# Kernel tuning notes

Measured on AMD Instinct MI355X. Metric: run time of the kernel, lower is better.

The kernel has to match this reference:

```python
import jax, jax.numpy as jnp
import numpy as np
from jax import lax

D_MODEL = 768
D_INNER = 1536   # expand * d_model
D_STATE = 16
D_CONV = 4
DT_RANK = 48     # ceil(768/16)
BATCH, SEQLEN = 2, 1024


def silu(x):
    return x * jax.nn.sigmoid(x)


def causal_conv1d(x, w, b):
    # x: (B, L, d)  w: (d, K) depthwise  b: (d,)
    # matches torch Conv1d(groups=d, padding=K-1)[..., :L]
    K = w.shape[1]
    L = x.shape[1]
    xp = jnp.pad(x, ((0, 0), (K - 1, 0), (0, 0)))
    out = b
    for k in range(K):
        out = out + xp[:, k:k + L, :] * w[:, k]
    return out


def mamba_branch(xz, conv_w, conv_b, x_proj_w, dt_proj_w, dt_bias, A_log, D):
    # xz: (B, L, 2*d_inner); faithful to mamba_inner_fn_no_out_proj
    x, z = jnp.split(xz, 2, axis=-1)
    x = silu(causal_conv1d(x, conv_w, conv_b))
    x_dbl = x @ x_proj_w.T                                  # (B,L,dt_rank+2N)
    dt, Bc, Cc = jnp.split(x_dbl, [DT_RANK, DT_RANK + D_STATE], axis=-1)
    delta = jax.nn.softplus(dt @ dt_proj_w.T + dt_bias)     # (B,L,d)
    A = -jnp.exp(A_log)                                     # (d,N)
    dA = jnp.exp(delta[..., None] * A)                      # (B,L,d,N)
    dBx = (delta * x)[..., None] * Bc[:, :, None, :]        # (B,L,d,N)

    def step(h, inp):
        da, dbx = inp
        h = da * h + dbx
        return h, h

    h0 = jnp.zeros((x.shape[0], x.shape[2], D_STATE), x.dtype)
    _, hs = lax.scan(step, h0, (jnp.swapaxes(dA, 0, 1), jnp.swapaxes(dBx, 0, 1)))
    y = jnp.einsum('lbdn,bln->bld', hs, Cc) + x * D         # (B,L,d)
    return y * silu(z)


def setup_inputs() -> dict:
    key = jax.random.key(0)
    ks = jax.random.split(key, 16)
    d, dm, n, r, K = D_INNER, D_MODEL, D_STATE, DT_RANK, D_CONV
    A_log = jnp.log(jnp.broadcast_to(jnp.arange(1, n + 1, dtype=jnp.float32), (d, n)))
    # faithful dt bias init: inverse-softplus of log-uniform dt in [1e-3, 1e-1]
    def dt_bias(k):
        dt = jnp.exp(jax.random.uniform(k, (d,)) * (np.log(0.1) - np.log(0.001)) + np.log(0.001))
        dt = jnp.clip(dt, 1e-4)
        return dt + jnp.log(-jnp.expm1(-dt))
    return {
        'hidden_states': jax.random.normal(ks[0], (BATCH, SEQLEN, dm), jnp.float32),
        'in_proj_w': jax.random.normal(ks[1], (2 * d, dm), jnp.float32) / np.sqrt(dm),
        'conv_w': jax.random.normal(ks[2], (d, K), jnp.float32) / np.sqrt(K),
        'conv_b': jax.random.normal(ks[3], (d,), jnp.float32) * 0.02,
        'x_proj_w': jax.random.normal(ks[4], (r + 2 * n, d), jnp.float32) / np.sqrt(d),
        'dt_proj_w': jax.random.uniform(ks[5], (d, r), jnp.float32, -r ** -0.5, r ** -0.5),
        'dt_proj_b': dt_bias(ks[6]),
        'A_log': A_log,
        'D': jnp.ones((d,), jnp.float32),
        'conv_w_b': jax.random.normal(ks[7], (d, K), jnp.float32) / np.sqrt(K),
        'conv_b_b': jax.random.normal(ks[8], (d,), jnp.float32) * 0.02,
        'x_proj_w_b': jax.random.normal(ks[9], (r + 2 * n, d), jnp.float32) / np.sqrt(d),
        'dt_proj_w_b': jax.random.uniform(ks[10], (d, r), jnp.float32, -r ** -0.5, r ** -0.5),
        'dt_proj_b_b': dt_bias(ks[11]),
        'A_b_log': A_log,
        'D_b': jnp.ones((d,), jnp.float32),
        'out_proj_w': jax.random.normal(ks[12], (dm, d), jnp.float32) / np.sqrt(d),
    }


def reference(hidden_states, in_proj_w, conv_w, conv_b, x_proj_w, dt_proj_w, dt_proj_b,
              A_log, D, conv_w_b, conv_b_b, x_proj_w_b, dt_proj_w_b, dt_proj_b_b,
              A_b_log, D_b, out_proj_w):
    # bimamba v2: forward scan + backward (flipped) scan, summed, then out_proj
    xz = hidden_states @ in_proj_w.T                        # (B,L,2*d_inner)
    out_f = mamba_branch(xz, conv_w, conv_b, x_proj_w, dt_proj_w, dt_proj_b, A_log, D)
    out_r = mamba_branch(xz[:, ::-1, :], conv_w_b, conv_b_b, x_proj_w_b,
                         dt_proj_w_b, dt_proj_b_b, A_b_log, D_b)[:, ::-1, :]
    return (out_f + out_r) @ out_proj_w.T                   # (B,L,d_model)
```

## Files before the change

### kernel.cpp

```cpp
#include <hip/hip_runtime.h>
#include <hip/hip_bf16.h>

#define LL 1024
#define DI 1536
#define N2 3072
#define ML 2048

typedef __attribute__((ext_vector_type(8))) short short8;
typedef __attribute__((ext_vector_type(4))) float f4;
typedef __attribute__((ext_vector_type(4))) float f32x4;

__device__ __forceinline__ ushort f2bf(float f) {
  union { float f; unsigned u; } v; v.f = f;
  unsigned u = v.u;
  u += 0x7fffu + ((u >> 16) & 1u);
  return (ushort)(u >> 16);
}
__device__ __forceinline__ float bf2f(ushort u) {
  union { unsigned i; float f; } w; w.i = ((unsigned)u) << 16; return w.f;
}

__device__ __forceinline__ void gload16(const ushort* g, ushort* l) {
  __builtin_amdgcn_global_load_lds(
      (const __attribute__((address_space(1))) unsigned int*)g,
      (__attribute__((address_space(3))) unsigned int*)l, 16, 0, 0);
}

struct CvtSeg { const float* s; ushort* d; int n4; };
struct Cvt5 { CvtSeg seg[5]; };

#define CVT_BLOCKS 5232

__global__ void k_cvt(Cvt5 p, int total4,
                      const float* __restrict__ wf, const float* __restrict__ wb,
                      ushort* __restrict__ dtw) {
  int bid = blockIdx.x;
  if (bid < CVT_BLOCKS) {
    int i = bid * 256 + threadIdx.x;
    if (i >= total4) return;
    int off = i, sidx = 0;
    while (sidx < 4 && off >= p.seg[sidx].n4) { off -= p.seg[sidx].n4; ++sidx; }
    f4 v = *(const f4*)(p.seg[sidx].s + (size_t)off * 4);
    ushort4 o;
    o.x = f2bf(v.x); o.y = f2bf(v.y); o.z = f2bf(v.z); o.w = f2bf(v.w);
    *(ushort4*)(p.seg[sidx].d + (size_t)off * 4) = o;
  } else {
    int i = (bid - CVT_BLOCKS) * 256 + threadIdx.x;
    int c = i & 63;
    int rr = i >> 6;
    int dir = rr / 1536;
    int r = rr - dir * 1536;
    const float* w = dir ? wb : wf;
    dtw[i] = (c < 48) ? f2bf(w[r * 48 + c]) : (ushort)0;
  }
}

template<int EPI, bool NGUARD, int KS>
__global__ __launch_bounds__(256)
void k_gemm(const ushort* __restrict__ A, const ushort* __restrict__ Bm,
            float* __restrict__ C, int M, int N, int K,
            const float* __restrict__ bias, const float* __restrict__ bias2,
            size_t sA, size_t sB, size_t sC, size_t sKs, int kLen) {
  const int dir = blockIdx.z;
  A += (size_t)dir * sA;
  Bm += (size_t)dir * sB;
  C += (size_t)dir * sC;
  const float* bp = (EPI == 1) ? (dir ? bias2 : bias) : nullptr;

  int n0, kOff, kEnd;
  if (KS > 1) {
    int yb_ = blockIdx.y;
    int nt = yb_ / KS, ks = yb_ - nt * KS;
    n0 = nt * 128;
    kOff = ks * kLen;
    kEnd = kOff + kLen;
    C += (size_t)ks * sKs;
  } else {
    n0 = blockIdx.y * 128;
    kOff = 0;
    kEnd = K;
  }

  __shared__ ushort As[128 * 32];
  __shared__ ushort Bs[128 * 32];
  const int tid = threadIdx.x;
  const int m0 = blockIdx.x * 128;
  const int wv = tid >> 6;
  const int lane = tid & 63;
  const int wr = (wv >> 1) * 64;
  const int wc = (wv & 1) * 64;
  const int lr = lane & 15;
  const int lk = lane >> 4;
  f32x4 acc[4][4] = {};
  for (int k0 = kOff; k0 < kEnd; k0 += 32) {
    #pragma unroll
    for (int i = 0; i < 2; ++i) {
      int e = (tid + i * 256) * 8;
      int r = e >> 5;
      int c = e & 31;
      gload16(A + (size_t)(m0 + r) * K + k0 + c, &As[(i * 256 + wv * 64) * 8]);
      gload16(Bm + (size_t)(n0 + r) * K + k0 + c, &Bs[(i * 256 + wv * 64) * 8]);
    }
    __syncthreads();
    short8 af[4], bfr[4];
    #pragma unroll
    for (int m = 0; m < 4; ++m) af[m] = *(const short8*)(&As[(wr + m*16 + lr) * 32 + lk*8]);
    #pragma unroll
    for (int n = 0; n < 4; ++n) bfr[n] = *(const short8*)(&Bs[(wc + n*16 + lr) * 32 + lk*8]);
    #pragma unroll
    for (int m = 0; m < 4; ++m)
      #pragma unroll
      for (int n = 0; n < 4; ++n)
        acc[m][n] = __builtin_amdgcn_mfma_f32_16x16x32_bf16(af[m], bfr[n], acc[m][n], 0, 0, 0);
    __syncthreads();
  }
  #pragma unroll
  for (int m = 0; m < 4; ++m) {
    int gr = m0 + wr + m * 16 + lk * 4;
    #pragma unroll
    for (int n = 0; n < 4; ++n) {
      int gc = n0 + wc + n * 16 + lr;
      if (NGUARD && gc >= N) continue;
      #pragma unroll
      for (int r = 0; r < 4; ++r) {
        float v = acc[m][n][r];
        if (EPI == 1) {
          v += bp[gc];
          v = (v > 20.f) ? v : log1pf(__expf(v));
        }
        C[(size_t)(gr + r) * N + gc] = v;
      }
    }
  }
}

__global__ void k_xred(const float* __restrict__ partial,
                       float* __restrict__ dtBC, ushort* __restrict__ dtbf) {
  int i = blockIdx.x * 256 + threadIdx.x;
  int dir = i / 40960;
  int rem = i - dir * 40960;
  int row = rem / 20;
  int c4 = rem - row * 20;
  f4 s = {0.f, 0.f, 0.f, 0.f};
  #pragma unroll
  for (int ks = 0; ks < 8; ++ks) {
    f4 v = *(const f4*)(partial + (((size_t)(dir * 8 + ks) * 2048 + row) * 80 + c4 * 4));
    s.x += v.x; s.y += v.y; s.z += v.z; s.w += v.w;
  }
  *(f4*)(dtBC + ((size_t)dir * 163840 + (size_t)row * 80 + c4 * 4)) = s;
  if (c4 < 16) {
    ushort4 u;
    if (c4 < 12) { u.x = f2bf(s.x); u.y = f2bf(s.y); u.z = f2bf(s.z); u.w = f2bf(s.w); }
    else { u.x = 0; u.y = 0; u.z = 0; u.w = 0; }
    *(ushort4*)(dtbf + ((size_t)dir * 131072 + (size_t)row * 64 + c4 * 4)) = u;
  }
}

__global__ void k_ored(const float* __restrict__ part, float* __restrict__ out) {
  int i = blockIdx.x * 256 + threadIdx.x;
  f4 s = {0.f, 0.f, 0.f, 0.f};
  #pragma unroll
  for (int ks = 0; ks < 4; ++ks) {
    f4 v = *(const f4*)(part + (size_t)ks * 1572864 + (size_t)i * 4);
    s.x += v.x; s.y += v.y; s.z += v.z; s.w += v.w;
  }
  *(f4*)(out + (size_t)i * 4) = s;
}

#define CONV_R 8
__global__ __launch_bounds__(192)
void k_conv2(const float* __restrict__ xz,
             const float* __restrict__ wf, const float* __restrict__ bf_,
             const float* __restrict__ wb, const float* __restrict__ bb_,
             ushort* __restrict__ xcbf) {
  int d4 = blockIdx.z * 192 + threadIdx.x;
  int b = blockIdx.y;
  int l0 = blockIdx.x * CONV_R;
  int d = d4 * 4;
  f4 w0[4], w1[4];
  #pragma unroll
  for (int c = 0; c < 4; ++c) {
    w0[c] = *(const f4*)(wf + (size_t)d * 4 + c * 4);
    w1[c] = *(const f4*)(wb + (size_t)d * 4 + c * 4);
  }
  f4 bias0 = *(const f4*)(bf_ + d);
  f4 bias1 = *(const f4*)(bb_ + d);
  f4 win[CONV_R + 6];
  #pragma unroll
  for (int j = 0; j < CONV_R + 6; ++j) {
    int t = l0 - 3 + j;
    if (t >= 0 && t < LL) {
      win[j] = *(const f4*)(xz + ((size_t)(b * LL + t)) * N2 + d);
    } else {
      f4 z = {0.f, 0.f, 0.f, 0.f};
      win[j] = z;
    }
  }
  #pragma unroll
  for (int i = 0; i < CONV_R; ++i) {
    int l = l0 + i;
    float a0[4], a1[4];
    #pragma unroll
    for (int c = 0; c < 4; ++c) { a0[c] = bias0[c]; a1[c] = bias1[c]; }
    #pragma unroll
    for (int k = 0; k < 4; ++k) {
      f4 xv0 = win[i + k];
      f4 xv1 = win[i + 3 + k];
      #pragma unroll
      for (int c = 0; c < 4; ++c) {
        a0[c] += xv0[c] * w0[c][k];
        a1[c] += xv1[c] * w1[c][3 - k];
      }
    }
    ushort4 o0, o1;
    #pragma unroll
    for (int c = 0; c < 4; ++c) {
      a0[c] = a0[c] / (1.f + __expf(-a0[c]));
      a1[c] = a1[c] / (1.f + __expf(-a1[c]));
    }
    o0.x = f2bf(a0[0]); o0.y = f2bf(a0[1]); o0.z = f2bf(a0[2]); o0.w = f2bf(a0[3]);
    o1.x = f2bf(a1[0]); o1.y = f2bf(a1[1]); o1.z = f2bf(a1[2]); o1.w = f2bf(a1[3]);
    *(ushort4*)(xcbf + ((size_t)(b * LL + l)) * DI + d) = o0;
    *(ushort4*)(xcbf + ((size_t)(ML + b * LL + (LL - 1 - l))) * DI + d) = o1;
  }
}

__global__ __launch_bounds__(256)
void k_scan1(const float* __restrict__ delta_all,
             const ushort* __restrict__ xc_all,
             const float* __restrict__ dtBC_all,
             const float* __restrict__ Alog_f, const float* __restrict__ Alog_b,
             float* __restrict__ hL, float* __restrict__ P) {
  int dirb = blockIdx.z;
  int dir = dirb >> 1, b = dirb & 1;
  int ch = blockIdx.y;
  int tid = threadIdx.x;
  int lane = tid & 63;
  int wv = tid >> 6;
  int ns = lane >> 4;
  int dl_ = lane & 15;
  int d = blockIdx.x * 64 + wv * 16 + dl_;
  const float* Alog = dir ? Alog_b : Alog_f;
  float Av[4];
  #pragma unroll
  for (int j = 0; j < 4; ++j) Av[j] = -__expf(Alog[d * 16 + ns * 4 + j]);
  int l0 = ch * 64;
  size_t base = ((size_t)dir * ML + (size_t)b * LL + l0) * DI + d;
  const float* dptr = delta_all + base;
  const ushort* xptr = xc_all + base;
  const float* bc = dtBC_all + ((size_t)dir * ML + (size_t)b * LL + l0) * 80 + 48 + ns * 4;
  float h[4] = {0.f, 0.f, 0.f, 0.f};
  float p[4] = {1.f, 1.f, 1.f, 1.f};
  #pragma unroll 4
  for (int l = 0; l < 64; ++l) {
    float dl = dptr[(size_t)l * DI];
    float xv = bf2f(xptr[(size_t)l * DI]);
    f4 Bv = *(const f4*)(bc + l * 80);
    float dbx = dl * xv;
    #pragma unroll
    for (int j = 0; j < 4; ++j) {
      float dA = __expf(dl * Av[j]);
      h[j] = dA * h[j] + dbx * Bv[j];
      p[j] *= dA;
    }
  }
  size_t si = (((size_t)dirb * 1536 + d) * 16 + ch) * 16 + ns * 4;
  f4 hv = {h[0], h[1], h[2], h[3]};
  f4 pv = {p[0], p[1], p[2], p[3]};
  *(f4*)(hL + si) = hv;
  *(f4*)(P + si) = pv;
}

__global__ void k_comb(const float* __restrict__ hL, const float* __restrict__ P,
                       float* __restrict__ hIn) {
  int tid = blockIdx.x * 256 + threadIdx.x;
  int n = tid & 15;
  size_t c = tid >> 4;
  float h = 0.f;
  size_t base = c * 256 + n;
  #pragma unroll
  for (int ch = 0; ch < 16; ++ch) {
    hIn[base + ch * 16] = h;
    h = P[base + ch * 16] * h + hL[base + ch * 16];
  }
}

__global__ __launch_bounds__(256)
void k_scan2(const float* __restrict__ delta_all,
             const ushort* __restrict__ xc_all,
             const float* __restrict__ dtBC_all,
             const float* __restrict__ Alog_f, const float* __restrict__ Df,
             const float* __restrict__ Alog_b, const float* __restrict__ Db,
             const float* __restrict__ hIn,
             float* __restrict__ yf, float* __restrict__ yb) {
  int dirb = blockIdx.z;
  int dir = dirb >> 1, b = dirb & 1;
  int ch = blockIdx.y;
  int tid = threadIdx.x;
  int lane = tid & 63;
  int wv = tid >> 6;
  int ns = lane >> 4;
  int dl_ = lane & 15;
  int d = blockIdx.x * 64 + wv * 16 + dl_;
  const float* Alog = dir ? Alog_b : Alog_f;
  const float* Dp = dir ? Db : Df;
  float Av[4];
  #pragma unroll
  for (int j = 0; j < 4; ++j) Av[j] = -__expf(Alog[d * 16 + ns * 4 + j]);
  float Dvv = Dp[d];
  int l0 = ch * 64;
  size_t base = ((size_t)dir * ML + (size_t)b * LL + l0) * DI + d;
  const float* dptr = delta_all + base;
  const ushort* xptr = xc_all + base;
  const float* bc = dtBC_all + ((size_t)dir * ML + (size_t)b * LL + l0) * 80 + 48 + ns * 4;
  float* yo = dir ? yb : yf;
  size_t hi = (((size_t)dirb * 1536 + d) * 16 + ch) * 16 + ns * 4;
  f4 h0 = *(const f4*)(hIn + hi);
  float h[4] = {h0.x, h0.y, h0.z, h0.w};
  #pragma unroll 4
  for (int l = 0; l < 64; ++l) {
    float dl = dptr[(size_t)l * DI];
    float xv = bf2f(xptr[(size_t)l * DI]);
    f4 Bv = *(const f4*)(bc + l * 80);
    f4 Cv = *(const f4*)(bc + 16 + l * 80);
    float dbx = dl * xv;
    float pr = 0.f;
    #pragma unroll
    for (int j = 0; j < 4; ++j) {
      float dA = __expf(dl * Av[j]);
      h[j] = dA * h[j] + dbx * Bv[j];
      pr += h[j] * Cv[j];
    }
    pr += __shfl_xor(pr, 16);
    pr += __shfl_xor(pr, 32);
    if (ns == 0) {
      int gl = l0 + l;
      int lo = dir ? (LL - 1 - gl) : gl;
      yo[((size_t)b * LL + lo) * DI + d] = pr + xv * Dvv;
    }
  }
}

__global__ void k_gate(const float* __restrict__ a, const float* __restrict__ b,
                       const float* __restrict__ xz, ushort* __restrict__ o) {
  int i = blockIdx.x * 256 + threadIdx.x;
  int row = i / 384;
  int c4 = i - row * 384;
  f4 va = *(const f4*)(a + (size_t)i * 4);
  f4 vb = *(const f4*)(b + (size_t)i * 4);
  f4 vz = *(const f4*)(xz + (size_t)row * N2 + DI + c4 * 4);
  ushort4 u;
  float s0 = vz.x / (1.f + __expf(-vz.x));
  float s1 = vz.y / (1.f + __expf(-vz.y));
  float s2 = vz.z / (1.f + __expf(-vz.z));
  float s3 = vz.w / (1.f + __expf(-vz.w));
  u.x = f2bf((va.x + vb.x) * s0);
  u.y = f2bf((va.y + vb.y) * s1);
  u.z = f2bf((va.z + vb.z) * s2);
  u.w = f2bf((va.w + vb.w) * s3);
  *(ushort4*)(o + (size_t)i * 4) = u;
}

extern "C" void kernel_launch(void* const* d_in, const int* in_sizes, int n_in,
                              void* d_out, int out_size, void* d_ws, size_t ws_size,
                              hipStream_t stream) {
  const float* hidden      = (const float*)d_in[0];
  const float* in_proj_w   = (const float*)d_in[1];
  const float* conv_w      = (const float*)d_in[2];
  const float* conv_b      = (const float*)d_in[3];
  const float* x_proj_w    = (const float*)d_in[4];
  const float* dt_proj_w   = (const float*)d_in[5];
  const float* dt_proj_b   = (const float*)d_in[6];
  const float* A_log       = (const float*)d_in[7];
  const float* Dv          = (const float*)d_in[8];
  const float* conv_w_b    = (const float*)d_in[9];
  const float* conv_b_b    = (const float*)d_in[10];
  const float* x_proj_w_b  = (const float*)d_in[11];
  const float* dt_proj_w_b = (const float*)d_in[12];
  const float* dt_proj_b_b = (const float*)d_in[13];
  const float* A_b_log     = (const float*)d_in[14];
  const float* D_b         = (const float*)d_in[15];
  const float* out_proj_w  = (const float*)d_in[16];
  float* out = (float*)d_out;

  float* wsf   = (float*)d_ws;
  float* xz    = wsf;
  float* dtBC  = wsf + 6291456;
  float* delta = wsf + 6619136;
  float* yf    = wsf + 12910592;
  float* yb    = wsf + 16056320;
  ushort* wsb     = (ushort*)((char*)d_ws + 76808192);
  ushort* hid_bf  = wsb;
  ushort* win_bf  = wsb + 1572864;
  ushort* xw_bf   = wsb + 3932160;
  ushort* dtw_bf  = wsb + 4177920;
  ushort* wout_bf = wsb + 4374528;
  ushort* xc_bf   = wsb + 5554176;
  ushort* dt_bf   = wsb + 11845632;
  ushort* y_bf    = wsb + 12107776;
  if (ws_size < 107315200) return;

  float* xpart = yf;
  float* opart = delta;
  float* hL  = yf;
  float* P   = yb;
  float* hIn = (float*)y_bf;

  Cvt5 c5;
  c5.seg[0] = { hidden,      hid_bf,            1572864 / 4 };
  c5.seg[1] = { in_proj_w,   win_bf,            2359296 / 4 };
  c5.seg[2] = { x_proj_w,    xw_bf,             122880 / 4 };
  c5.seg[3] = { x_proj_w_b,  xw_bf + 122880,    122880 / 4 };
  c5.seg[4] = { out_proj_w,  wout_bf,           1179648 / 4 };
  k_cvt<<<CVT_BLOCKS + 768, 256, 0, stream>>>(c5, 1339392, dt_proj_w, dt_proj_w_b, dtw_bf);

  k_gemm<0, false, 1><<<dim3(16, 24), 256, 0, stream>>>(
      hid_bf, win_bf, xz, 2048, 3072, 768, nullptr, nullptr, 0, 0, 0, 0, 0);

  k_conv2<<<dim3(LL / CONV_R, 2, 2), 192, 0, stream>>>(
      xz, conv_w, conv_b, conv_w_b, conv_b_b, xc_bf);

  k_gemm<0, true, 8><<<dim3(16, 8, 2), 256, 0, stream>>>(
      xc_bf, xw_bf, xpart, 2048, 80, 1536, nullptr, nullptr,
      3145728, 122880, 1310720, 163840, 192);
  k_xred<<<320, 256, 0, stream>>>(xpart, dtBC, dt_bf);

  k_gemm<1, false, 1><<<dim3(16, 12, 2), 256, 0, stream>>>(
      dt_bf, dtw_bf, delta, 2048, 1536, 64, dt_proj_b, dt_proj_b_b,
      131072, 98304, 3145728, 0, 0);

  k_scan1<<<dim3(24, 16, 4), 256, 0, stream>>>(delta, xc_bf, dtBC, A_log, A_b_log, hL, P);
  k_comb<<<384, 256, 0, stream>>>(hL, P, hIn);
  k_scan2<<<dim3(24, 16, 4), 256, 0, stream>>>(delta, xc_bf, dtBC,
                                               A_log, Dv, A_b_log, D_b, hIn, yf, yb);

  k_gate<<<3072, 256, 0, stream>>>(yf, yb, xz, y_bf);

  k_gemm<0, false, 4><<<dim3(16, 24), 256, 0, stream>>>(
      y_bf, wout_bf, opart, 2048, 768, 1536, nullptr, nullptr,
      0, 0, 0, 1572864, 384);
  k_ored<<<1536, 256, 0, stream>>>(opart, out);
}
```

Baseline: 281.8 us.

## Store xz, delta and scan outputs as bf16 and compute chunk decay from delta sum

The in_proj GEMM and the dt_proj GEMM now write bf16 instead of fp32. The conv, scan and gate kernels read these bf16 intermediates, and the scan2 outputs are also stored as bf16. The goal is to roughly halve memory traffic on the large intermediate tensors and shrink the workspace layout. Separately, scan1 stops multiplying a per-state decay product each step. It accumulates the sum of delta and computes exp(A*sum) once at the end, which saves a multiply per state per step. The cost is lower precision in delta, xz and y, which could affect accuracy.

```diff
diff --git a/kernel.cpp b/kernel.cpp
--- a/kernel.cpp
+++ b/kernel.cpp
@@ -18,6 +18,10 @@
 }
 __device__ __forceinline__ float bf2f(ushort u) {
   union { unsigned i; float f; } w; w.i = ((unsigned)u) << 16; return w.f;
+}
+__device__ __forceinline__ f4 bf2f4(ushort4 u) {
+  f4 r; r.x = bf2f(u.x); r.y = bf2f(u.y); r.z = bf2f(u.z); r.w = bf2f(u.w);
+  return r;
 }
 
 __device__ __forceinline__ void gload16(const ushort* g, ushort* l) {
@@ -55,16 +59,16 @@
   }
 }
 
-template<int EPI, bool NGUARD, int KS>
+template<int EPI, bool NGUARD, int KS, bool OBF>
 __global__ __launch_bounds__(256)
 void k_gemm(const ushort* __restrict__ A, const ushort* __restrict__ Bm,
-            float* __restrict__ C, int M, int N, int K,
+            void* __restrict__ Cp, int M, int N, int K,
             const float* __restrict__ bias, const float* __restrict__ bias2,
             size_t sA, size_t sB, size_t sC, size_t sKs, int kLen) {
   const int dir = blockIdx.z;
   A += (size_t)dir * sA;
   Bm += (size_t)dir * sB;
-  C += (size_t)dir * sC;
+  size_t cbase = (size_t)dir * sC;
   const float* bp = (EPI == 1) ? (dir ? bias2 : bias) : nullptr;
 
   int n0, kOff, kEnd;
@@ -74,7 +78,7 @@
     n0 = nt * 128;
     kOff = ks * kLen;
     kEnd = kOff + kLen;
-    C += (size_t)ks * sKs;
+    cbase += (size_t)ks * sKs;
   } else {
     n0 = blockIdx.y * 128;
     kOff = 0;
@@ -128,7 +132,9 @@
           v += bp[gc];
           v = (v > 20.f) ? v : log1pf(__expf(v));
         }
-        C[(size_t)(gr + r) * N + gc] = v;
+        size_t idx = cbase + (size_t)(gr + r) * N + gc;
+        if (OBF) ((ushort*)Cp)[idx] = f2bf(v);
+        else     ((float*)Cp)[idx] = v;
       }
     }
   }
@@ -169,7 +175,7 @@
 
 #define CONV_R 8
 __global__ __launch_bounds__(192)
-void k_conv2(const float* __restrict__ xz,
+void k_conv2(const ushort* __restrict__ xz,
              const float* __restrict__ wf, const float* __restrict__ bf_,
              const float* __restrict__ wb, const float* __restrict__ bb_,
              ushort* __restrict__ xcbf) {
@@ -190,7 +196,7 @@
   for (int j = 0; j < CONV_R + 6; ++j) {
     int t = l0 - 3 + j;
     if (t >= 0 && t < LL) {
-      win[j] = *(const f4*)(xz + ((size_t)(b * LL + t)) * N2 + d);
+      win[j] = bf2f4(*(const ushort4*)(xz + ((size_t)(b * LL + t)) * N2 + d));
     } else {
       f4 z = {0.f, 0.f, 0.f, 0.f};
       win[j] = z;
@@ -226,7 +232,7 @@
 }
 
 __global__ __launch_bounds__(256)
-void k_scan1(const float* __restrict__ delta_all,
+void k_scan1(const ushort* __restrict__ delta_all,
              const ushort* __restrict__ xc_all,
              const float* __restrict__ dtBC_all,
              const float* __restrict__ Alog_f, const float* __restrict__ Alog_b,
@@ -246,27 +252,27 @@
   for (int j = 0; j < 4; ++j) Av[j] = -__expf(Alog[d * 16 + ns * 4 + j]);
   int l0 = ch * 64;
   size_t base = ((size_t)dir * ML + (size_t)b * LL + l0) * DI + d;
-  const float* dptr = delta_all + base;
+  const ushort* dptr = delta_all + base;
   const ushort* xptr = xc_all + base;
   const float* bc = dtBC_all + ((size_t)dir * ML + (size_t)b * LL + l0) * 80 + 48 + ns * 4;
   float h[4] = {0.f, 0.f, 0.f, 0.f};
-  float p[4] = {1.f, 1.f, 1.f, 1.f};
+  float s = 0.f;
   #pragma unroll 4
   for (int l = 0; l < 64; ++l) {
-    float dl = dptr[(size_t)l * DI];
+    float dl = bf2f(dptr[(size_t)l * DI]);
     float xv = bf2f(xptr[(size_t)l * DI]);
     f4 Bv = *(const f4*)(bc + l * 80);
     float dbx = dl * xv;
+    s += dl;
     #pragma unroll
     for (int j = 0; j < 4; ++j) {
       float dA = __expf(dl * Av[j]);
       h[j] = dA * h[j] + dbx * Bv[j];
-      p[j] *= dA;
     }
   }
   size_t si = (((size_t)dirb * 1536 + d) * 16 + ch) * 16 + ns * 4;
   f4 hv = {h[0], h[1], h[2], h[3]};
-  f4 pv = {p[0], p[1], p[2], p[3]};
+  f4 pv = {__expf(Av[0] * s), __expf(Av[1] * s), __expf(Av[2] * s), __expf(Av[3] * s)};
   *(f4*)(hL + si) = hv;
   *(f4*)(P + si) = pv;
 }
@@ -286,13 +292,13 @@
 }
 
 __global__ __launch_bounds__(256)
-void k_scan2(const float* __restrict__ delta_all,
+void k_scan2(const ushort* __restrict__ delta_all,
              const ushort* __restrict__ xc_all,
              const float* __restrict__ dtBC_all,
              const float* __restrict__ Alog_f, const float* __restrict__ Df,
              const float* __restrict__ Alog_b, const float* __restrict__ Db,
              const float* __restrict__ hIn,
-             float* __restrict__ yf, float* __restrict__ yb) {
+             ushort* __restrict__ yf, ushort* __restrict__ yb) {
   int dirb = blockIdx.z;
   int dir = dirb >> 1, b = dirb & 1;
   int ch = blockIdx.y;
@@ -310,16 +316,16 @@
   float Dvv = Dp[d];
   int l0 = ch * 64;
   size_t base = ((size_t)dir * ML + (size_t)b * LL + l0) * DI + d;
-  const float* dptr = delta_all + base;
+  const ushort* dptr = delta_all + base;
   const ushort* xptr = xc_all + base;
   const float* bc = dtBC_all + ((size_t)dir * ML + (size_t)b * LL + l0) * 80 + 48 + ns * 4;
-  float* yo = dir ? yb : yf;
+  ushort* yo = dir ? yb : yf;
   size_t hi = (((size_t)dirb * 1536 + d) * 16 + ch) * 16 + ns * 4;
   f4 h0 = *(const f4*)(hIn + hi);
   float h[4] = {h0.x, h0.y, h0.z, h0.w};
   #pragma unroll 4
   for (int l = 0; l < 64; ++l) {
-    float dl = dptr[(size_t)l * DI];
+    float dl = bf2f(dptr[(size_t)l * DI]);
     float xv = bf2f(xptr[(size_t)l * DI]);
     f4 Bv = *(const f4*)(bc + l * 80);
     f4 Cv = *(const f4*)(bc + 16 + l * 80);
@@ -336,19 +342,19 @@
     if (ns == 0) {
       int gl = l0 + l;
       int lo = dir ? (LL - 1 - gl) : gl;
-      yo[((size_t)b * LL + lo) * DI + d] = pr + xv * Dvv;
-    }
-  }
-}
-
-__global__ void k_gate(const float* __restrict__ a, const float* __restrict__ b,
-                       const float* __restrict__ xz, ushort* __restrict__ o) {
+      yo[((size_t)b * LL + lo) * DI + d] = f2bf(pr + xv * Dvv);
+    }
+  }
+}
+
+__global__ void k_gate(const ushort* __restrict__ a, const ushort* __restrict__ b,
+                       const ushort* __restrict__ xz, ushort* __restrict__ o) {
   int i = blockIdx.x * 256 + threadIdx.x;
   int row = i / 384;
   int c4 = i - row * 384;
-  f4 va = *(const f4*)(a + (size_t)i * 4);
-  f4 vb = *(const f4*)(b + (size_t)i * 4);
-  f4 vz = *(const f4*)(xz + (size_t)row * N2 + DI + c4 * 4);
+  f4 va = bf2f4(*(const ushort4*)(a + (size_t)i * 4));
+  f4 vb = bf2f4(*(const ushort4*)(b + (size_t)i * 4));
+  f4 vz = bf2f4(*(const ushort4*)(xz + (size_t)row * N2 + DI + c4 * 4));
   ushort4 u;
   float s0 = vz.x / (1.f + __expf(-vz.x));
   float s1 = vz.y / (1.f + __expf(-vz.y));
@@ -384,27 +390,26 @@
   float* out = (float*)d_out;
 
   float* wsf   = (float*)d_ws;
-  float* xz    = wsf;
-  float* dtBC  = wsf + 6291456;
-  float* delta = wsf + 6619136;
-  float* yf    = wsf + 12910592;
-  float* yb    = wsf + 16056320;
-  ushort* wsb     = (ushort*)((char*)d_ws + 76808192);
-  ushort* hid_bf  = wsb;
-  ushort* win_bf  = wsb + 1572864;
-  ushort* xw_bf   = wsb + 3932160;
-  ushort* dtw_bf  = wsb + 4177920;
-  ushort* wout_bf = wsb + 4374528;
-  ushort* xc_bf   = wsb + 5554176;
-  ushort* dt_bf   = wsb + 11845632;
-  ushort* y_bf    = wsb + 12107776;
-  if (ws_size < 107315200) return;
-
-  float* xpart = yf;
-  float* opart = delta;
-  float* hL  = yf;
-  float* P   = yb;
-  float* hIn = (float*)y_bf;
+  float* dtBC  = wsf;
+  float* hL    = wsf + 327680;
+  float* P     = wsf + 1900544;
+  float* hIn   = wsf + 3473408;
+  float* xpart = wsf + 327680;
+  float* opart = wsf;
+  ushort* wsb      = (ushort*)((char*)d_ws + 25165824);
+  ushort* hid_bf   = wsb;
+  ushort* win_bf   = wsb + 1572864;
+  ushort* xw_bf    = wsb + 3932160;
+  ushort* dtw_bf   = wsb + 4177920;
+  ushort* wout_bf  = wsb + 4374528;
+  ushort* xz_bf    = wsb + 5554176;
+  ushort* xc_bf    = wsb + 11845632;
+  ushort* dt_bf    = wsb + 18137088;
+  ushort* delta_bf = wsb + 18399232;
+  ushort* ybf_f    = wsb + 24690688;
+  ushort* ybf_b    = wsb + 27836416;
+  ushort* y_bf     = wsb + 30982144;
+  if (ws_size < 93421568) return;
 
   Cvt5 c5;
   c5.seg[0] = { hidden,      hid_bf,            1572864 / 4 };
@@ -414,29 +419,29 @@
   c5.seg[4] = { out_proj_w,  wout_bf,           1179648 / 4 };
   k_cvt<<<CVT_BLOCKS + 768, 256, 0, stream>>>(c5, 1339392, dt_proj_w, dt_proj_w_b, dtw_bf);
 
-  k_gemm<0, false, 1><<<dim3(16, 24), 256, 0, stream>>>(
-      hid_bf, win_bf, xz, 2048, 3072, 768, nullptr, nullptr, 0, 0, 0, 0, 0);
+  k_gemm<0, false, 1, true><<<dim3(16, 24), 256, 0, stream>>>(
+      hid_bf, win_bf, xz_bf, 2048, 3072, 768, nullptr, nullptr, 0, 0, 0, 0, 0);
 
   k_conv2<<<dim3(LL / CONV_R, 2, 2), 192, 0, stream>>>(
-      xz, conv_w, conv_b, conv_w_b, conv_b_b, xc_bf);
-
-  k_gemm<0, true, 8><<<dim3(16, 8, 2), 256, 0, stream>>>(
+      xz_bf, conv_w, conv_b, conv_w_b, conv_b_b, xc_bf);
+
+  k_gemm<0, true, 8, false><<<dim3(16, 8, 2), 256, 0, stream>>>(
       xc_bf, xw_bf, xpart, 2048, 80, 1536, nullptr, nullptr,
       3145728, 122880, 1310720, 163840, 192);
   k_xred<<<320, 256, 0, stream>>>(xpart, dtBC, dt_bf);
 
-  k_gemm<1, false, 1><<<dim3(16, 12, 2), 256, 0, stream>>>(
-      dt_bf, dtw_bf, delta, 2048, 1536, 64, dt_proj_b, dt_proj_b_b,
+  k_gemm<1, false, 1, true><<<dim3(16, 12, 2), 256, 0, stream>>>(
+      dt_bf, dtw_bf, delta_bf, 2048, 1536, 64, dt_proj_b, dt_proj_b_b,
       131072, 98304, 3145728, 0, 0);
 
-  k_scan1<<<dim3(24, 16, 4), 256, 0, stream>>>(delta, xc_bf, dtBC, A_log, A_b_log, hL, P);
+  k_scan1<<<dim3(24, 16, 4), 256, 0, stream>>>(delta_bf, xc_bf, dtBC, A_log, A_b_log, hL, P);
   k_comb<<<384, 256, 0, stream>>>(hL, P, hIn);
-  k_scan2<<<dim3(24, 16, 4), 256, 0, stream>>>(delta, xc_bf, dtBC,
-                                               A_log, Dv, A_b_log, D_b, hIn, yf, yb);
-
-  k_gate<<<3072, 256, 0, stream>>>(yf, yb, xz, y_bf);
-
-  k_gemm<0, false, 4><<<dim3(16, 24), 256, 0, stream>>>(
+  k_scan2<<<dim3(24, 16, 4), 256, 0, stream>>>(delta_bf, xc_bf, dtBC,
+                                               A_log, Dv, A_b_log, D_b, hIn, ybf_f, ybf_b);
+
+  k_gate<<<3072, 256, 0, stream>>>(ybf_f, ybf_b, xz_bf, y_bf);
+
+  k_gemm<0, false, 4, false><<<dim3(16, 24), 256, 0, stream>>>(
       y_bf, wout_bf, opart, 2048, 768, 1536, nullptr, nullptr,
       0, 0, 0, 1572864, 384);
   k_ored<<<1536, 256, 0, stream>>>(opart, out);
```

Result: no change. 277.2 us (-1.6%).
